# Kernel tuning notes

Hardware: AMD Instinct MI355X
Metric: run time of the kernel (lower is better)

## Reference

```python
import jax, jax.numpy as jnp
import numpy as np

MARGIN = 1.0
BIG = 1e4  # larger than any cosine distance (max 2.0)

def setup_inputs() -> dict:
    key = jax.random.key(0)
    k1, k2 = jax.random.split(key)
    embeddings = jax.random.normal(k1, (4096, 512), dtype=jnp.float32)
    labels = jax.random.randint(k2, (4096,), 0, 512, dtype=jnp.int64)
    return {"embeddings": embeddings, "labels": labels}

def reference(embeddings, labels):
    b = embeddings.shape[0]
    # L2-normalize rows (torch F.normalize uses eps=1e-12 clamp on norm)
    norms = jnp.linalg.norm(embeddings, axis=1, keepdims=True)
    emb_n = embeddings / jnp.maximum(norms, 1e-12)
    sim = emb_n @ emb_n.T                      # [b, b]
    dist = jnp.maximum(1.0 - sim, 0.0)         # cosine distance, clamped at 0

    same = labels[:, None] == labels[None, :]  # [b, b]
    eye = jnp.eye(b, dtype=bool)
    pos_mask = same & ~eye
    neg_mask = ~same

    # batch-hard mining: row-wise masked max over positives, min over negatives
    hardest_pos = jnp.max(jnp.where(pos_mask, dist, 0.0), axis=1)   # dist >= 0 so 0 is neutral for max
    hardest_neg = jnp.min(jnp.where(neg_mask, dist, BIG), axis=1)

    valid = jnp.any(pos_mask, axis=1) & jnp.any(neg_mask, axis=1)
    per_row = jax.nn.relu(hardest_pos - hardest_neg + MARGIN)
    loss_sum = jnp.sum(jnp.where(valid, per_row, 0.0))
    num_valid = jnp.sum(valid)
    return loss_sum / jnp.maximum(num_valid, 1).astype(loss_sum.dtype)
```

## Files before the change

kernel.cpp:

```cpp
#include <hip/hip_runtime.h>
#include <hip/hip_bf16.h>

#define BATCH 4096
#define DIM   512
#define NLBL  512
#define BIGF  1e4f
#define MARGIN 1.0f

#define BM 128
#define BK 32
#define NT (BATCH/BM)
#define NPAIR (NT*(NT+1)/2)
#define KITERS (DIM/BK)

using f32x4  = __attribute__((ext_vector_type(4))) float;
using bf16x8 = __attribute__((ext_vector_type(8))) short;

__device__ __forceinline__ unsigned short f2bf(float x) {
    __hip_bfloat16 h = __float2bfloat16(x);
    return *reinterpret_cast<unsigned short*>(&h);
}

#define GLOAD16(gp, lp) \
    __builtin_amdgcn_global_load_lds((const __attribute__((address_space(1))) void*)(gp), \
                                     (__attribute__((address_space(3))) void*)(lp), 16, 0, 0)

__global__ __launch_bounds__(256) void normalize_k(const float* __restrict__ emb,
                                                   unsigned short* __restrict__ Hi,
                                                   unsigned* __restrict__ hp,
                                                   unsigned* __restrict__ hn) {
    int wave = threadIdx.x >> 6;
    int lane = threadIdx.x & 63;
    int row  = blockIdx.x * 4 + wave;
    const float4* src = (const float4*)(emb + (size_t)row * DIM);
    float4 v0 = src[lane * 2];
    float4 v1 = src[lane * 2 + 1];
    float ss = v0.x*v0.x + v0.y*v0.y + v0.z*v0.z + v0.w*v0.w
             + v1.x*v1.x + v1.y*v1.y + v1.z*v1.z + v1.w*v1.w;
    #pragma unroll
    for (int off = 1; off < 64; off <<= 1) ss += __shfl_xor(ss, off);
    float scale = 1.0f / fmaxf(sqrtf(ss), 1e-12f);
    bf16x8 o;
    o[0] = (short)f2bf(v0.x * scale);
    o[1] = (short)f2bf(v0.y * scale);
    o[2] = (short)f2bf(v0.z * scale);
    o[3] = (short)f2bf(v0.w * scale);
    o[4] = (short)f2bf(v1.x * scale);
    o[5] = (short)f2bf(v1.y * scale);
    o[6] = (short)f2bf(v1.z * scale);
    o[7] = (short)f2bf(v1.w * scale);
    *(bf16x8*)(Hi + (size_t)row * DIM + lane * 8) = o;
    if (lane == 0) {
        hp[row] = 0u;
        hn[row] = __float_as_uint(BIGF);
    }
}

__global__ __launch_bounds__(256, 4) void mine_k(const unsigned short* __restrict__ Hi,
                                                 const int* __restrict__ lab,
                                                 unsigned* __restrict__ hp,
                                                 unsigned* __restrict__ hn) {
    __shared__ __attribute__((aligned(16))) unsigned short As[2][BM * BK];
    __shared__ __attribute__((aligned(16))) unsigned short Bs[2][BM * BK];
    __shared__ float rowp[2][BM], rown[2][BM], colp[2][BM], coln[2][BM];

    int p = (int)blockIdx.x;
    p = (p & 7) * (NPAIR / 8) + (p >> 3);
    int bi = 0, rem = p;
    while (rem >= NT - bi) { rem -= NT - bi; ++bi; }
    int bj = bi + rem;
    const int i0 = bi * BM;
    const int j0 = bj * BM;

    const int tid  = threadIdx.x;
    const int w    = tid >> 6;
    const int lane = tid & 63;
    const int wr   = w >> 1;
    const int wc   = w & 1;
    const int l15  = lane & 15;
    const int lhi  = lane >> 4;

    f32x4 acc[4][4] = {};
    const char* HiB = (const char*)Hi;

    auto STAGE = [&](int buf, int t) {
        const size_t kb = (size_t)t * (BK * 2);
        #pragma unroll
        for (int q = 0; q < 2; ++q) {
            int r16 = w * 32 + q * 16;
            int lr  = r16 + (lane >> 2);
            int sc  = (lane & 3) ^ ((lr >> 1) & 3);
            const char* ga = HiB + (size_t)(i0 + lr) * (DIM * 2) + kb + (sc << 4);
            const char* gb = HiB + (size_t)(j0 + lr) * (DIM * 2) + kb + (sc << 4);
            GLOAD16(ga, (char*)As[buf] + r16 * 64);
            GLOAD16(gb, (char*)Bs[buf] + r16 * 64);
        }
    };
    auto COMPUTE = [&](int buf) {
        bf16x8 a[4], b[4];
        #pragma unroll
        for (int m = 0; m < 4; ++m) {
            int row = wr * 64 + m * 16 + l15;
            int cp  = lhi ^ ((row >> 1) & 3);
            a[m] = *(const bf16x8*)((const char*)As[buf] + row * 64 + (cp << 4));
        }
        #pragma unroll
        for (int n = 0; n < 4; ++n) {
            int row = wc * 64 + n * 16 + l15;
            int cp  = lhi ^ ((row >> 1) & 3);
            b[n] = *(const bf16x8*)((const char*)Bs[buf] + row * 64 + (cp << 4));
        }
        #pragma unroll
        for (int m = 0; m < 4; ++m)
            #pragma unroll
            for (int n = 0; n < 4; ++n)
                acc[m][n] = __builtin_amdgcn_mfma_f32_16x16x32_bf16(a[m], b[n], acc[m][n], 0, 0, 0);
    };

    STAGE(0, 0);
    STAGE(1, 1);
    #pragma unroll
    for (int t = 0; t < KITERS; ++t) {
        const int cur = t & 1;
        if (t < KITERS - 1) {
            asm volatile("s_waitcnt vmcnt(4)" ::: "memory");
        } else {
            asm volatile("s_waitcnt vmcnt(0)" ::: "memory");
        }
        __builtin_amdgcn_sched_barrier(0);
        __builtin_amdgcn_s_barrier();
        COMPUTE(cur);
        __builtin_amdgcn_sched_barrier(0);
        __builtin_amdgcn_s_barrier();
        if (t + 2 < KITERS) STAGE(cur, t + 2);
    }

    int lj[4];
    #pragma unroll
    for (int n = 0; n < 4; ++n) lj[n] = lab[j0 + wc * 64 + n * 16 + l15];
    int li[16];
    #pragma unroll
    for (int m = 0; m < 4; ++m)
        #pragma unroll
        for (int r = 0; r < 4; ++r)
            li[m * 4 + r] = lab[i0 + wr * 64 + m * 16 + lhi * 4 + r];

    #pragma unroll
    for (int m = 0; m < 4; ++m) {
        #pragma unroll
        for (int r = 0; r < 4; ++r) {
            int i   = i0 + wr * 64 + m * 16 + lhi * 4 + r;
            int lir = li[m * 4 + r];
            float pm = 0.0f, nm = BIGF;
            #pragma unroll
            for (int n = 0; n < 4; ++n) {
                float dist = fmaxf(1.0f - acc[m][n][r], 0.0f);
                int j = j0 + wc * 64 + n * 16 + l15;
                if (lir == lj[n]) {
                    if (i != j) pm = fmaxf(pm, dist);
                } else {
                    nm = fminf(nm, dist);
                }
            }
            #pragma unroll
            for (int off = 1; off < 16; off <<= 1) {
                pm = fmaxf(pm, __shfl_xor(pm, off));
                nm = fminf(nm, __shfl_xor(nm, off));
            }
            if (l15 == 0) {
                int loc = wr * 64 + m * 16 + lhi * 4 + r;
                rowp[wc][loc] = pm;
                rown[wc][loc] = nm;
            }
        }
    }

    #pragma unroll
    for (int n = 0; n < 4; ++n) {
        int j   = j0 + wc * 64 + n * 16 + l15;
        int ljn = lj[n];
        float cp = 0.0f, cn = BIGF;
        #pragma unroll
        for (int m = 0; m < 4; ++m) {
            #pragma unroll
            for (int r = 0; r < 4; ++r) {
                float dist = fmaxf(1.0f - acc[m][n][r], 0.0f);
                int i = i0 + wr * 64 + m * 16 + lhi * 4 + r;
                if (li[m * 4 + r] == ljn) {
                    if (i != j) cp = fmaxf(cp, dist);
                } else {
                    cn = fminf(cn, dist);
                }
            }
        }
        #pragma unroll
        for (int off = 16; off < 64; off <<= 1) {
            cp = fmaxf(cp, __shfl_xor(cp, off));
            cn = fminf(cn, __shfl_xor(cn, off));
        }
        if (lhi == 0) {
            int loc = wc * 64 + n * 16 + l15;
            colp[wr][loc] = cp;
            coln[wr][loc] = cn;
        }
    }

    __syncthreads();

    if (tid < BM) {
        float pmv = fmaxf(rowp[0][tid], rowp[1][tid]);
        float nmv = fminf(rown[0][tid], rown[1][tid]);
        atomicMax(hp + i0 + tid, __float_as_uint(pmv));
        atomicMin(hn + i0 + tid, __float_as_uint(nmv));
    } else {
        int c = tid - BM;
        float pmv = fmaxf(colp[0][c], colp[1][c]);
        float nmv = fminf(coln[0][c], coln[1][c]);
        atomicMax(hp + j0 + c, __float_as_uint(pmv));
        atomicMin(hn + j0 + c, __float_as_uint(nmv));
    }
}

__global__ __launch_bounds__(1024) void final_k(const int* __restrict__ lab,
                                                const unsigned* __restrict__ hp,
                                                const unsigned* __restrict__ hn,
                                                float* __restrict__ out) {
    __shared__ int   cnt[NLBL];
    __shared__ float ssum[16];
    __shared__ int   scnt[16];
    int t = threadIdx.x;
    for (int i = t; i < NLBL; i += 1024) cnt[i] = 0;
    __syncthreads();
    for (int i = t; i < BATCH; i += 1024) atomicAdd(&cnt[lab[i]], 1);
    __syncthreads();

    float lsum = 0.0f;
    int   lcnt = 0;
    for (int i = t; i < BATCH; i += 1024) {
        int c = cnt[lab[i]];
        if ((c > 1) && (c < BATCH)) {
            float per = fmaxf(__uint_as_float(hp[i]) - __uint_as_float(hn[i]) + MARGIN, 0.0f);
            lsum += per;
            lcnt += 1;
        }
    }
    #pragma unroll
    for (int off = 1; off < 64; off <<= 1) {
        lsum += __shfl_xor(lsum, off);
        lcnt += __shfl_xor(lcnt, off);
    }
    int w = t >> 6;
    if ((t & 63) == 0) { ssum[w] = lsum; scnt[w] = lcnt; }
    __syncthreads();
    if (t == 0) {
        float s = 0.0f; int c2 = 0;
        #pragma unroll
        for (int i = 0; i < 16; ++i) { s += ssum[i]; c2 += scnt[i]; }
        out[0] = s / (float)max(c2, 1);
    }
}

extern "C" void kernel_launch(void* const* d_in, const int* in_sizes, int n_in,
                              void* d_out, int out_size, void* d_ws, size_t ws_size,
                              hipStream_t stream) {
    const float* emb = (const float*)d_in[0];
    const int*   lab = (const int*)d_in[1];

    char* base = (char*)d_ws;
    unsigned short* Hi = (unsigned short*)base;
    unsigned* hp = (unsigned*)(base + (size_t)BATCH * DIM * 2);
    unsigned* hn = hp + BATCH;

    normalize_k<<<BATCH / 4, 256, 0, stream>>>(emb, Hi, hp, hn);
    mine_k<<<NPAIR, 256, 0, stream>>>(Hi, lab, hp, hn);
    final_k<<<1, 1024, 0, stream>>>(lab, hp, hn, (float*)d_out);
}
```

Measured before the change: 36.37 us.

## Give each wave an independent 64x64 tile pair with barrier-free pipelining

```diff
diff --git a/kernel.cpp b/kernel.cpp
--- a/kernel.cpp
+++ b/kernel.cpp
@@ -7,10 +7,11 @@
 #define BIGF  1e4f
 #define MARGIN 1.0f
 
-#define BM 128
+#define BM 64
 #define BK 32
 #define NT (BATCH/BM)
 #define NPAIR (NT*(NT+1)/2)
+#define NBLK (NPAIR/2)
 #define KITERS (DIM/BK)
 
 using f32x4  = __attribute__((ext_vector_type(4))) float;
@@ -56,65 +57,44 @@
     }
 }
 
-__global__ __launch_bounds__(256, 4) void mine_k(const unsigned short* __restrict__ Hi,
+__global__ __launch_bounds__(128, 4) void mine_k(const unsigned short* __restrict__ Hi,
                                                  const int* __restrict__ lab,
                                                  unsigned* __restrict__ hp,
                                                  unsigned* __restrict__ hn) {
-    __shared__ __attribute__((aligned(16))) unsigned short As[2][BM * BK];
-    __shared__ __attribute__((aligned(16))) unsigned short Bs[2][BM * BK];
-    __shared__ float rowp[2][BM], rown[2][BM], colp[2][BM], coln[2][BM];
-
-    int p = (int)blockIdx.x;
-    p = (p & 7) * (NPAIR / 8) + (p >> 3);
+    __shared__ __attribute__((aligned(16))) unsigned short As[2][2][BM * BK];
+    __shared__ __attribute__((aligned(16))) unsigned short Bs[2][2][BM * BK];
+
+    const int tid  = threadIdx.x;
+    const int w    = tid >> 6;
+    const int lane = tid & 63;
+    const int l15  = lane & 15;
+    const int lhi  = lane >> 4;
+
+    int bb = (int)blockIdx.x;
+    bb = (bb & 7) * (NBLK / 8) + (bb >> 3);
+    int p = bb * 2 + w;
     int bi = 0, rem = p;
     while (rem >= NT - bi) { rem -= NT - bi; ++bi; }
     int bj = bi + rem;
     const int i0 = bi * BM;
     const int j0 = bj * BM;
 
-    const int tid  = threadIdx.x;
-    const int w    = tid >> 6;
-    const int lane = tid & 63;
-    const int wr   = w >> 1;
-    const int wc   = w & 1;
-    const int l15  = lane & 15;
-    const int lhi  = lane >> 4;
-
     f32x4 acc[4][4] = {};
     const char* HiB = (const char*)Hi;
+    unsigned short (*A)[BM * BK] = As[w];
+    unsigned short (*B)[BM * BK] = Bs[w];
 
     auto STAGE = [&](int buf, int t) {
         const size_t kb = (size_t)t * (BK * 2);
         #pragma unroll
-        for (int q = 0; q < 2; ++q) {
-            int r16 = w * 32 + q * 16;
-            int lr  = r16 + (lane >> 2);
-            int sc  = (lane & 3) ^ ((lr >> 1) & 3);
+        for (int q = 0; q < 4; ++q) {
+            int lr = q * 16 + (lane >> 2);
+            int sc = (lane & 3) ^ ((lr >> 1) & 3);
             const char* ga = HiB + (size_t)(i0 + lr) * (DIM * 2) + kb + (sc << 4);
             const char* gb = HiB + (size_t)(j0 + lr) * (DIM * 2) + kb + (sc << 4);
-            GLOAD16(ga, (char*)As[buf] + r16 * 64);
-            GLOAD16(gb, (char*)Bs[buf] + r16 * 64);
-        }
-    };
-    auto COMPUTE = [&](int buf) {
-        bf16x8 a[4], b[4];
-        #pragma unroll
-        for (int m = 0; m < 4; ++m) {
-            int row = wr * 64 + m * 16 + l15;
-            int cp  = lhi ^ ((row >> 1) & 3);
-            a[m] = *(const bf16x8*)((const char*)As[buf] + row * 64 + (cp << 4));
-        }
-        #pragma unroll
-        for (int n = 0; n < 4; ++n) {
-            int row = wc * 64 + n * 16 + l15;
-            int cp  = lhi ^ ((row >> 1) & 3);
-            b[n] = *(const bf16x8*)((const char*)Bs[buf] + row * 64 + (cp << 4));
-        }
-        #pragma unroll
-        for (int m = 0; m < 4; ++m)
-            #pragma unroll
-            for (int n = 0; n < 4; ++n)
-                acc[m][n] = __builtin_amdgcn_mfma_f32_16x16x32_bf16(a[m], b[n], acc[m][n], 0, 0, 0);
+            GLOAD16(ga, (char*)A[buf] + q * 1024);
+            GLOAD16(gb, (char*)B[buf] + q * 1024);
+        }
     };
 
     STAGE(0, 0);
@@ -123,39 +103,57 @@
     for (int t = 0; t < KITERS; ++t) {
         const int cur = t & 1;
         if (t < KITERS - 1) {
-            asm volatile("s_waitcnt vmcnt(4)" ::: "memory");
+            asm volatile("s_waitcnt vmcnt(8)" ::: "memory");
         } else {
             asm volatile("s_waitcnt vmcnt(0)" ::: "memory");
         }
         __builtin_amdgcn_sched_barrier(0);
-        __builtin_amdgcn_s_barrier();
-        COMPUTE(cur);
+
+        bf16x8 a[4], b[4];
+        #pragma unroll
+        for (int m = 0; m < 4; ++m) {
+            int row = m * 16 + l15;
+            int cp  = lhi ^ ((row >> 1) & 3);
+            a[m] = *(const bf16x8*)((const char*)A[cur] + row * 64 + (cp << 4));
+        }
+        #pragma unroll
+        for (int n = 0; n < 4; ++n) {
+            int row = n * 16 + l15;
+            int cp  = lhi ^ ((row >> 1) & 3);
+            b[n] = *(const bf16x8*)((const char*)B[cur] + row * 64 + (cp << 4));
+        }
+        asm volatile("s_waitcnt lgkmcnt(0)" ::: "memory");
         __builtin_amdgcn_sched_barrier(0);
-        __builtin_amdgcn_s_barrier();
         if (t + 2 < KITERS) STAGE(cur, t + 2);
+
+        #pragma unroll
+        for (int m = 0; m < 4; ++m)
+            #pragma unroll
+            for (int n = 0; n < 4; ++n)
+                acc[m][n] = __builtin_amdgcn_mfma_f32_16x16x32_bf16(a[m], b[n], acc[m][n], 0, 0, 0);
     }
 
     int lj[4];
     #pragma unroll
-    for (int n = 0; n < 4; ++n) lj[n] = lab[j0 + wc * 64 + n * 16 + l15];
+    for (int n = 0; n < 4; ++n) lj[n] = lab[j0 + n * 16 + l15];
     int li[16];
     #pragma unroll
     for (int m = 0; m < 4; ++m)
         #pragma unroll
         for (int r = 0; r < 4; ++r)
-            li[m * 4 + r] = lab[i0 + wr * 64 + m * 16 + lhi * 4 + r];
+            li[m * 4 + r] = lab[i0 + m * 16 + lhi * 4 + r];
 
     #pragma unroll
     for (int m = 0; m < 4; ++m) {
         #pragma unroll
         for (int r = 0; r < 4; ++r) {
-            int i   = i0 + wr * 64 + m * 16 + lhi * 4 + r;
+            int i   = i0 + m * 16 + lhi * 4 + r;
             int lir = li[m * 4 + r];
             float pm = 0.0f, nm = BIGF;
             #pragma unroll
             for (int n = 0; n < 4; ++n) {
                 float dist = fmaxf(1.0f - acc[m][n][r], 0.0f);
-                int j = j0 + wc * 64 + n * 16 + l15;
+                int j = j0 + n * 16 + l15;
                 if (lir == lj[n]) {
                     if (i != j) pm = fmaxf(pm, dist);
                 } else {
@@ -168,16 +166,15 @@
                 nm = fminf(nm, __shfl_xor(nm, off));
             }
             if (l15 == 0) {
-                int loc = wr * 64 + m * 16 + lhi * 4 + r;
-                rowp[wc][loc] = pm;
-                rown[wc][loc] = nm;
+                atomicMax(hp + i, __float_as_uint(pm));
+                atomicMin(hn + i, __float_as_uint(nm));
             }
         }
     }
 
     #pragma unroll
     for (int n = 0; n < 4; ++n) {
-        int j   = j0 + wc * 64 + n * 16 + l15;
+        int j   = j0 + n * 16 + l15;
         int ljn = lj[n];
         float cp = 0.0f, cn = BIGF;
         #pragma unroll
@@ -185,7 +182,7 @@
             #pragma unroll
             for (int r = 0; r < 4; ++r) {
                 float dist = fmaxf(1.0f - acc[m][n][r], 0.0f);
-                int i = i0 + wr * 64 + m * 16 + lhi * 4 + r;
+                int i = i0 + m * 16 + lhi * 4 + r;
                 if (li[m * 4 + r] == ljn) {
                     if (i != j) cp = fmaxf(cp, dist);
                 } else {
@@ -199,25 +196,9 @@
             cn = fminf(cn, __shfl_xor(cn, off));
         }
         if (lhi == 0) {
-            int loc = wc * 64 + n * 16 + l15;
-            colp[wr][loc] = cp;
-            coln[wr][loc] = cn;
-        }
-    }
-
-    __syncthreads();
-
-    if (tid < BM) {
-        float pmv = fmaxf(rowp[0][tid], rowp[1][tid]);
-        float nmv = fminf(rown[0][tid], rown[1][tid]);
-        atomicMax(hp + i0 + tid, __float_as_uint(pmv));
-        atomicMin(hn + i0 + tid, __float_as_uint(nmv));
-    } else {
-        int c = tid - BM;
-        float pmv = fmaxf(colp[0][c], colp[1][c]);
-        float nmv = fminf(coln[0][c], coln[1][c]);
-        atomicMax(hp + j0 + c, __float_as_uint(pmv));
-        atomicMin(hn + j0 + c, __float_as_uint(nmv));
+            atomicMax(hp + j, __float_as_uint(cp));
+            atomicMin(hn + j, __float_as_uint(cn));
+        }
     }
 }
 
@@ -272,6 +253,6 @@
     unsigned* hn = hp + BATCH;
 
     normalize_k<<<BATCH / 4, 256, 0, stream>>>(emb, Hi, hp, hn);
-    mine_k<<<NPAIR, 256, 0, stream>>>(Hi, lab, hp, hn);
+    mine_k<<<NBLK, 128, 0, stream>>>(Hi, lab, hp, hn);
     final_k<<<1, 1024, 0, stream>>>(lab, hp, hn, (float*)d_out);
 }
```

After: 47.69 us. 31.1% more time.
